# Optimization experiments

Measured on AMD Instinct MI355X. Metric: run time of the kernel, lower is better.

The kernel has to match this reference:

```python
import jax, jax.numpy as jnp
import numpy as np

B, S, D, H = 2, 2048, 1024, 16
DK = D // H


def setup_inputs() -> dict:
    key = jax.random.key(0)
    ks = jax.random.split(key, 7)
    q = jax.random.normal(ks[0], (B, S, D), dtype=jnp.float32)
    k = jax.random.normal(ks[1], (B, S, D), dtype=jnp.float32)
    v = jax.random.normal(ks[2], (B, S, D), dtype=jnp.float32)
    # causal mask (1 = keep, 0 = mask) broadcast over batch/heads
    mask = jnp.tril(jnp.ones((S, S), dtype=jnp.int32))[None, None, :, :]
    scale = 1.0 / np.sqrt(DK)
    W_q = jax.random.normal(ks[3], (D, D), dtype=jnp.float32) * 0.02
    W_k = jax.random.normal(ks[4], (D, D), dtype=jnp.float32) * 0.02
    W_v = jax.random.normal(ks[5], (D, D), dtype=jnp.float32) * 0.02
    W_o = jax.random.normal(ks[6], (D, D), dtype=jnp.float32) * 0.02
    return {"q": q, "k": k, "v": v, "mask": mask,
            "W_q": W_q, "W_k": W_k, "W_v": W_v, "W_o": W_o}


def _split_heads(x):
    # [B, S, D] -> [B, H, S, DK]
    b, s, _ = x.shape
    return x.reshape(b, s, H, DK).transpose(0, 2, 1, 3)


def reference(q, k, v, mask, W_q, W_k, W_v, W_o):
    # nn.Linear(bias=False): y = x @ W.T
    qh = _split_heads(q @ W_q.T)
    kh = _split_heads(k @ W_k.T)
    vh = _split_heads(v @ W_v.T)
    scores = jnp.einsum("bhqd,bhkd->bhqk", qh, kh) / np.sqrt(DK)
    scores = jnp.where(mask == 0, jnp.float32(-1e9), scores)
    attn = jax.nn.softmax(scores, axis=-1)  # dropout p=0 -> identity
    out = jnp.einsum("bhqk,bhkd->bhqd", attn, vh)
    out = out.transpose(0, 2, 1, 3).reshape(q.shape[0], q.shape[1], D)
    return out @ W_o.T
```

## Files before the change

### kernel.cpp

```cpp
#include <hip/hip_runtime.h>
#include <stdint.h>
#include <stddef.h>

typedef __bf16 bf16;
typedef __attribute__((ext_vector_type(4))) __bf16 bf16x4;
typedef __attribute__((ext_vector_type(8))) __bf16 bf16x8;
typedef __attribute__((ext_vector_type(4))) float floatx4;

#define NB 2
#define NS 2048
#define ND 1024
#define NH 16
#define NDK 64
#define NBH (NB*NH)
#define NBS (NB*NS)

__device__ inline void gl2lds16(const bf16* g, bf16* l) {
  __builtin_amdgcn_global_load_lds(
      (const __attribute__((address_space(1))) uint32_t*)(const uint32_t*)(g),
      (__attribute__((address_space(3))) uint32_t*)(uint32_t*)(l),
      16, 0, 0);
}

__global__ __launch_bounds__(256)
void proj_gemm(const float* __restrict__ q, const float* __restrict__ k,
               const float* __restrict__ v,
               const float* __restrict__ Wq, const float* __restrict__ Wk,
               const float* __restrict__ Wv,
               bf16* __restrict__ Qh, bf16* __restrict__ Kh,
               bf16* __restrict__ Vt)
{
  const int z = blockIdx.y, bx = blockIdx.x;
  const int tid = threadIdx.x;
  const int wave = tid >> 6, lane = tid & 63;
  const int quad = lane >> 4, l15 = lane & 15;

  const float *X, *W;
  int m0, n0;
  if (z < 2) { X = z ? k : q;  W = z ? Wk : Wq;
               m0 = (bx >> 3) * 128; n0 = (bx & 7) * 128; }
  else       { X = Wv;         W = v;
               m0 = (bx & 7) * 128;  n0 = (bx >> 3) * 128; }

  __shared__ bf16 As[128 * 32];
  __shared__ bf16 Bs[128 * 32];

  float4 ra[4], rb[4];
#pragma unroll
  for (int it = 0; it < 4; it++) {
    const int lin = it * 256 + tid, row = lin >> 3, ch = lin & 7;
    ra[it] = *(const float4*)(X + (size_t)(m0 + row) * ND + ch * 4);
    rb[it] = *(const float4*)(W + (size_t)(n0 + row) * ND + ch * 4);
  }

  floatx4 acc[4][4];
#pragma unroll
  for (int i = 0; i < 4; i++)
#pragma unroll
    for (int j = 0; j < 4; j++) acc[i][j] = (floatx4)(0.0f);

  const int wm = (wave >> 1) * 64, wn = (wave & 1) * 64;

  for (int k0 = 0; k0 < ND; k0 += 32) {
    __syncthreads();
#pragma unroll
    for (int it = 0; it < 4; it++) {
      const int lin = it * 256 + tid, row = lin >> 3, ch = lin & 7;
      bf16x4 a, b;
      a[0] = (bf16)ra[it].x; a[1] = (bf16)ra[it].y;
      a[2] = (bf16)ra[it].z; a[3] = (bf16)ra[it].w;
      b[0] = (bf16)rb[it].x; b[1] = (bf16)rb[it].y;
      b[2] = (bf16)rb[it].z; b[3] = (bf16)rb[it].w;
      *(bf16x4*)(As + row * 32 + ch * 4) = a;
      *(bf16x4*)(Bs + row * 32 + ch * 4) = b;
    }
    __syncthreads();
    if (k0 + 32 < ND) {
      const int k1 = k0 + 32;
#pragma unroll
      for (int it = 0; it < 4; it++) {
        const int lin = it * 256 + tid, row = lin >> 3, ch = lin & 7;
        ra[it] = *(const float4*)(X + (size_t)(m0 + row) * ND + k1 + ch * 4);
        rb[it] = *(const float4*)(W + (size_t)(n0 + row) * ND + k1 + ch * 4);
      }
    }
    bf16x8 af[4], bfr[4];
#pragma unroll
    for (int i = 0; i < 4; i++)
      af[i] = *(const bf16x8*)(As + (wm + i * 16 + l15) * 32 + quad * 8);
#pragma unroll
    for (int j = 0; j < 4; j++)
      bfr[j] = *(const bf16x8*)(Bs + (wn + j * 16 + l15) * 32 + quad * 8);
#pragma unroll
    for (int i = 0; i < 4; i++)
#pragma unroll
      for (int j = 0; j < 4; j++)
        acc[i][j] = __builtin_amdgcn_mfma_f32_16x16x32_bf16(af[i], bfr[j],
                                                            acc[i][j], 0, 0, 0);
  }

  bf16* O = (z == 0) ? Qh : (z == 1) ? Kh : Vt;
#pragma unroll
  for (int i = 0; i < 4; i++) {
    const int rowb = m0 + wm + i * 16 + quad * 4;
#pragma unroll
    for (int j = 0; j < 4; j++) {
      const int col = n0 + wn + j * 16 + l15;
#pragma unroll
      for (int r = 0; r < 4; r++) {
        const int row = rowb + r;
        const bf16 o = (bf16)acc[i][j][r];
        if (z < 2) {
          const int b = row >> 11, s = row & 2047;
          const int h = col >> 6,  dk = col & 63;
          O[(((size_t)(b * NH + h)) * NS + s) * NDK + dk] = o;
        } else {
          O[((size_t)(col >> 11) * ND + row) * NS + (col & 2047)] = o;
        }
      }
    }
  }
}

__global__ __launch_bounds__(256)
void attn_fwd(const bf16* __restrict__ Qh, const bf16* __restrict__ Kh,
              const bf16* __restrict__ Vt, bf16* __restrict__ Ctx)
{
  const int x = blockIdx.x, bh = blockIdx.y;
  const int tid = threadIdx.x, wave = tid >> 6, lane = tid & 63;
  const int quad = lane >> 4, l15 = lane & 15;

  __shared__ bf16 Ks[2][64 * 64];
  __shared__ bf16 Vs[2][64 * 64];
  __shared__ bf16 Ps[4][16 * 64];

  const size_t qkb = (size_t)bh * NS * NDK;
  const size_t vb  = (size_t)bh * NDK * NS;
  const int b = bh >> 4, h = bh & 15;
  const float C = 0.125f * 1.44269504088896f;

  auto stage = [&](int kt, int buf) {
#pragma unroll
    for (int it = 0; it < 2; it++) {
      const int lin = it * 256 + tid;
      const int row = lin >> 3;
      const int chS = (lin & 7) ^ (row & 7);
      gl2lds16(Kh + qkb + (size_t)(kt * 64 + row) * NDK + chS * 8,
               Ks[buf] + lin * 8);
      gl2lds16(Vt + vb + (size_t)row * NS + kt * 64 + chS * 8,
               Vs[buf] + lin * 8);
    }
  };

  for (int ph = 0; ph < 2; ph++) {
    const int qt = ph ? x : 31 - x;
    const int qrow0 = qt * 64 + wave * 16;

    bf16x8 qf0, qf1;
    {
      const bf16* qp = Qh + qkb + (size_t)(qrow0 + l15) * NDK + quad * 8;
      qf0 = *(const bf16x8*)qp;
      qf1 = *(const bf16x8*)(qp + 32);
    }

    float lsum[4] = {0.0f, 0.0f, 0.0f, 0.0f};
    floatx4 oacc[4];
#pragma unroll
    for (int j = 0; j < 4; j++) oacc[j] = (floatx4)(0.0f);

    __syncthreads();
    stage(0, 0);

    for (int kt = 0; kt <= qt; kt++) {
      const int cur = kt & 1;
      __builtin_amdgcn_s_waitcnt(0);
      __syncthreads();
      if (kt < qt) stage(kt + 1, cur ^ 1);

      const bf16* Ksb = Ks[cur];
      const bf16* Vsb = Vs[cur];

      floatx4 sa[4];
#pragma unroll
      for (int jt = 0; jt < 4; jt++) {
        const int r = jt * 16 + l15;
        const bf16x8 kf0 = *(const bf16x8*)(Ksb + r * 64 + ((quad ^ (r & 7)) << 3));
        const bf16x8 kf1 = *(const bf16x8*)(Ksb + r * 64 + (((4 + quad) ^ (r & 7)) << 3));
        floatx4 zz = (floatx4)(0.0f);
        zz = __builtin_amdgcn_mfma_f32_16x16x32_bf16(qf0, kf0, zz, 0, 0, 0);
        zz = __builtin_amdgcn_mfma_f32_16x16x32_bf16(qf1, kf1, zz, 0, 0, 0);
        sa[jt] = zz;
      }

      const bool diag = (kt == qt);
#pragma unroll
      for (int jt = 0; jt < 4; jt++) {
        const int col = jt * 16 + l15;
#pragma unroll
        for (int r = 0; r < 4; r++) {
          const int row = quad * 4 + r;
          float p = exp2f(sa[jt][r] * C);
          if (diag) p = (kt * 64 + col <= qrow0 + row) ? p : 0.0f;
          lsum[r] += p;
          Ps[wave][row * 64 + ((((col >> 3) ^ (row & 7))) << 3) + (col & 7)] =
              (bf16)p;
        }
      }

#pragma unroll
      for (int ks = 0; ks < 2; ks++) {
        const bf16x8 pf = *(const bf16x8*)(
            &Ps[wave][l15 * 64 + (((ks * 4 + quad) ^ (l15 & 7)) << 3)]);
#pragma unroll
        for (int jt = 0; jt < 4; jt++) {
          const int r = jt * 16 + l15;
          const bf16x8 vf = *(const bf16x8*)(
              Vsb + r * 64 + (((ks * 4 + quad) ^ (r & 7)) << 3));
          oacc[jt] = __builtin_amdgcn_mfma_f32_16x16x32_bf16(pf, vf,
                                                             oacc[jt], 0, 0, 0);
        }
      }
    }

#pragma unroll
    for (int off = 1; off < 16; off <<= 1)
#pragma unroll
      for (int r = 0; r < 4; r++) lsum[r] += __shfl_xor(lsum[r], off, 64);

#pragma unroll
    for (int jt = 0; jt < 4; jt++)
#pragma unroll
      for (int r = 0; r < 4; r++) {
        const int srow = qrow0 + quad * 4 + r;
        Ctx[((size_t)b * NS + srow) * ND + h * 64 + jt * 16 + l15] =
            (bf16)(oacc[jt][r] / lsum[r]);
      }
  }
}

__global__ __launch_bounds__(256)
void out_gemm(const bf16* __restrict__ Ctx, const float* __restrict__ Wo,
              float* __restrict__ out)
{
  const int tid = threadIdx.x;
  const int wave = tid >> 6, lane = tid & 63;
  const int quad = lane >> 4, l15 = lane & 15;
  const int m0 = blockIdx.y * 64, n0 = blockIdx.x * 128;
  const int wm = (wave & 1) * 32, wn = (wave >> 1) * 64;

  __shared__ bf16 As[64 * 32];
  __shared__ bf16 Bs[128 * 32];

  bf16x8 ra;
  float4 rb[4];
  {
    const int row = tid >> 2, ch = tid & 3;
    ra = *(const bf16x8*)(Ctx + (size_t)(m0 + row) * ND + ch * 8);
  }
#pragma unroll
  for (int it = 0; it < 4; it++) {
    const int lin = it * 256 + tid, row = lin >> 3, ch = lin & 7;
    rb[it] = *(const float4*)(Wo + (size_t)(n0 + row) * ND + ch * 4);
  }

  floatx4 acc[2][4];
#pragma unroll
  for (int i = 0; i < 2; i++)
#pragma unroll
    for (int j = 0; j < 4; j++) acc[i][j] = (floatx4)(0.0f);

  for (int k0 = 0; k0 < ND; k0 += 32) {
    __syncthreads();
    {
      const int row = tid >> 2, ch = tid & 3;
      *(bf16x8*)(As + row * 32 + ch * 8) = ra;
    }
#pragma unroll
    for (int it = 0; it < 4; it++) {
      const int lin = it * 256 + tid, row = lin >> 3, ch = lin & 7;
      bf16x4 bb;
      bb[0] = (bf16)rb[it].x; bb[1] = (bf16)rb[it].y;
      bb[2] = (bf16)rb[it].z; bb[3] = (bf16)rb[it].w;
      *(bf16x4*)(Bs + row * 32 + ch * 4) = bb;
    }
    __syncthreads();
    if (k0 + 32 < ND) {
      const int k1 = k0 + 32;
      {
        const int row = tid >> 2, ch = tid & 3;
        ra = *(const bf16x8*)(Ctx + (size_t)(m0 + row) * ND + k1 + ch * 8);
      }
#pragma unroll
      for (int it = 0; it < 4; it++) {
        const int lin = it * 256 + tid, row = lin >> 3, ch = lin & 7;
        rb[it] = *(const float4*)(Wo + (size_t)(n0 + row) * ND + k1 + ch * 4);
      }
    }
    bf16x8 af[2], bfr[4];
#pragma unroll
    for (int i = 0; i < 2; i++)
      af[i] = *(const bf16x8*)(As + (wm + i * 16 + l15) * 32 + quad * 8);
#pragma unroll
    for (int j = 0; j < 4; j++)
      bfr[j] = *(const bf16x8*)(Bs + (wn + j * 16 + l15) * 32 + quad * 8);
#pragma unroll
    for (int i = 0; i < 2; i++)
#pragma unroll
      for (int j = 0; j < 4; j++)
        acc[i][j] = __builtin_amdgcn_mfma_f32_16x16x32_bf16(af[i], bfr[j],
                                                            acc[i][j], 0, 0, 0);
  }

#pragma unroll
  for (int i = 0; i < 2; i++) {
    const int rowb = m0 + wm + i * 16 + quad * 4;
#pragma unroll
    for (int j = 0; j < 4; j++) {
      const int col = n0 + wn + j * 16 + l15;
#pragma unroll
      for (int r = 0; r < 4; r++)
        out[(size_t)(rowb + r) * ND + col] = acc[i][j][r];
    }
  }
}

extern "C" void kernel_launch(void* const* d_in, const int* in_sizes, int n_in,
                              void* d_out, int out_size, void* d_ws, size_t ws_size,
                              hipStream_t stream) {
  const float* q  = (const float*)d_in[0];
  const float* k  = (const float*)d_in[1];
  const float* v  = (const float*)d_in[2];
  const float* Wq = (const float*)d_in[4];
  const float* Wk = (const float*)d_in[5];
  const float* Wv = (const float*)d_in[6];
  const float* Wo = (const float*)d_in[7];
  float* out = (float*)d_out;

  const size_t elems = (size_t)NBS * ND;
  bf16* Qh  = (bf16*)d_ws;
  bf16* Kh  = Qh + elems;
  bf16* Vt  = Kh + elems;
  bf16* Ctx = Vt + elems;

  dim3 blk(256);
  proj_gemm<<<dim3(256, 3), blk, 0, stream>>>(q, k, v, Wq, Wk, Wv, Qh, Kh, Vt);
  attn_fwd<<<dim3(16, NBH), blk, 0, stream>>>(Qh, Kh, Vt, Ctx);
  out_gemm<<<dim3(ND / 128, NBS / 64), blk, 0, stream>>>(Ctx, Wo, out);
}
```

Measured before the change: 258.8 us.

## Pre-convert weights to bf16 and double-buffer GEMM tiles with direct LDS loads

A new kernel converts Wq/Wk/Wv to bf16 once, into workspace that aliases the Ctx buffer. The projection GEMM then streams that bf16 weight tile straight into shared memory with global_load_lds, while the fp32 activation tile is converted in registers. Both projection and output GEMMs now double-buffer their shared tiles so each K step needs one barrier instead of two. They also remap block indices for better L2 locality, and the V projection no longer swaps operands. The costs are an extra kernel launch, extra weight traffic through the workspace, and twice the shared memory per block.

New measurement: 275.8 us. 1.07x slower.

```diff
diff --git a/kernel.cpp b/kernel.cpp
--- a/kernel.cpp
+++ b/kernel.cpp
@@ -23,10 +23,31 @@
 }
 
 __global__ __launch_bounds__(256)
+void convert_w(const float* __restrict__ Wq, const float* __restrict__ Wk,
+               const float* __restrict__ Wv, bf16* __restrict__ Wb)
+{
+  const int z = blockIdx.y;
+  const float* src = (z == 0) ? Wq : (z == 1) ? Wk : Wv;
+  bf16* dst = Wb + (size_t)z * (ND * ND);
+  const size_t off = ((size_t)blockIdx.x * 256 + threadIdx.x) * 32;
+#pragma unroll
+  for (int c = 0; c < 2; c++) {
+    bf16x8 o[2];
+#pragma unroll
+    for (int h = 0; h < 2; h++) {
+      const float4 a = *(const float4*)(src + off + c * 16 + h * 8);
+      const float4 b = *(const float4*)(src + off + c * 16 + h * 8 + 4);
+      o[h][0] = (bf16)a.x; o[h][1] = (bf16)a.y; o[h][2] = (bf16)a.z; o[h][3] = (bf16)a.w;
+      o[h][4] = (bf16)b.x; o[h][5] = (bf16)b.y; o[h][6] = (bf16)b.z; o[h][7] = (bf16)b.w;
+    }
+    *(bf16x8*)(dst + off + c * 16) = o[0];
+    *(bf16x8*)(dst + off + c * 16 + 8) = o[1];
+  }
+}
+
+__global__ __launch_bounds__(256)
 void proj_gemm(const float* __restrict__ q, const float* __restrict__ k,
-               const float* __restrict__ v,
-               const float* __restrict__ Wq, const float* __restrict__ Wk,
-               const float* __restrict__ Wv,
+               const float* __restrict__ v, const bf16* __restrict__ Wb,
                bf16* __restrict__ Qh, bf16* __restrict__ Kh,
                bf16* __restrict__ Vt)
 {
@@ -35,62 +56,76 @@
   const int wave = tid >> 6, lane = tid & 63;
   const int quad = lane >> 4, l15 = lane & 15;
 
-  const float *X, *W;
-  int m0, n0;
-  if (z < 2) { X = z ? k : q;  W = z ? Wk : Wq;
-               m0 = (bx >> 3) * 128; n0 = (bx & 7) * 128; }
-  else       { X = Wv;         W = v;
-               m0 = (bx & 7) * 128;  n0 = (bx >> 3) * 128; }
-
-  __shared__ bf16 As[128 * 32];
-  __shared__ bf16 Bs[128 * 32];
-
-  float4 ra[4], rb[4];
+  const float* X = (z == 0) ? q : (z == 1) ? k : v;
+  const bf16* W = Wb + (size_t)z * (ND * ND);
+  const int c = bx & 7, r = bx >> 3;
+  const int m0 = (c * 4 + (r >> 3)) * 128, n0 = (r & 7) * 128;
+
+  __shared__ bf16 As[2][128 * 32];
+  __shared__ bf16 Bs[2][128 * 32];
+
+  const int arow = tid >> 3, ach = tid & 7;
+  const int brow = tid >> 2, bch = tid & 3;
+
+  floatx4 acc[4][4];
+#pragma unroll
+  for (int i = 0; i < 4; i++)
+#pragma unroll
+    for (int j = 0; j < 4; j++) acc[i][j] = (floatx4)(0.0f);
+
+  const int wm = (wave >> 1) * 64, wn = (wave & 1) * 64;
+
+  float4 ra[4];
+#pragma unroll
+  for (int it = 0; it < 4; it++)
+    ra[it] = *(const float4*)(X + (size_t)(m0 + it * 32 + arow) * ND + ach * 4);
+#pragma unroll
+  for (int it = 0; it < 2; it++)
+    gl2lds16(W + (size_t)(n0 + it * 64 + brow) * ND + bch * 8,
+             Bs[0] + (it * 256 + tid) * 8);
+  __builtin_amdgcn_s_waitcnt(0);
 #pragma unroll
   for (int it = 0; it < 4; it++) {
-    const int lin = it * 256 + tid, row = lin >> 3, ch = lin & 7;
-    ra[it] = *(const float4*)(X + (size_t)(m0 + row) * ND + ch * 4);
-    rb[it] = *(const float4*)(W + (size_t)(n0 + row) * ND + ch * 4);
-  }
-
-  floatx4 acc[4][4];
-#pragma unroll
-  for (int i = 0; i < 4; i++)
-#pragma unroll
-    for (int j = 0; j < 4; j++) acc[i][j] = (floatx4)(0.0f);
-
-  const int wm = (wave >> 1) * 64, wn = (wave & 1) * 64;
-
-  for (int k0 = 0; k0 < ND; k0 += 32) {
+    bf16x4 a;
+    a[0] = (bf16)ra[it].x; a[1] = (bf16)ra[it].y;
+    a[2] = (bf16)ra[it].z; a[3] = (bf16)ra[it].w;
+    *(bf16x4*)(As[0] + (it * 32 + arow) * 32 + ach * 4) = a;
+  }
+#pragma unroll
+  for (int it = 0; it < 4; it++)
+    ra[it] = *(const float4*)(X + (size_t)(m0 + it * 32 + arow) * ND + 32 + ach * 4);
+
+  for (int kk = 0; kk < 32; kk++) {
+    const int cur = kk & 1, nxt = cur ^ 1;
+    __builtin_amdgcn_s_waitcnt(0);
     __syncthreads();
-#pragma unroll
-    for (int it = 0; it < 4; it++) {
-      const int lin = it * 256 + tid, row = lin >> 3, ch = lin & 7;
-      bf16x4 a, b;
-      a[0] = (bf16)ra[it].x; a[1] = (bf16)ra[it].y;
-      a[2] = (bf16)ra[it].z; a[3] = (bf16)ra[it].w;
-      b[0] = (bf16)rb[it].x; b[1] = (bf16)rb[it].y;
-      b[2] = (bf16)rb[it].z; b[3] = (bf16)rb[it].w;
-      *(bf16x4*)(As + row * 32 + ch * 4) = a;
-      *(bf16x4*)(Bs + row * 32 + ch * 4) = b;
-    }
-    __syncthreads();
-    if (k0 + 32 < ND) {
-      const int k1 = k0 + 32;
+    if (kk + 1 < 32) {
+      const int k1 = (kk + 1) * 32;
+#pragma unroll
+      for (int it = 0; it < 2; it++)
+        gl2lds16(W + (size_t)(n0 + it * 64 + brow) * ND + k1 + bch * 8,
+                 Bs[nxt] + (it * 256 + tid) * 8);
 #pragma unroll
       for (int it = 0; it < 4; it++) {
-        const int lin = it * 256 + tid, row = lin >> 3, ch = lin & 7;
-        ra[it] = *(const float4*)(X + (size_t)(m0 + row) * ND + k1 + ch * 4);
-        rb[it] = *(const float4*)(W + (size_t)(n0 + row) * ND + k1 + ch * 4);
+        bf16x4 a;
+        a[0] = (bf16)ra[it].x; a[1] = (bf16)ra[it].y;
+        a[2] = (bf16)ra[it].z; a[3] = (bf16)ra[it].w;
+        *(bf16x4*)(As[nxt] + (it * 32 + arow) * 32 + ach * 4) = a;
+      }
+      if (kk + 2 < 32) {
+        const int k2 = (kk + 2) * 32;
+#pragma unroll
+        for (int it = 0; it < 4; it++)
+          ra[it] = *(const float4*)(X + (size_t)(m0 + it * 32 + arow) * ND + k2 + ach * 4);
       }
     }
     bf16x8 af[4], bfr[4];
 #pragma unroll
     for (int i = 0; i < 4; i++)
-      af[i] = *(const bf16x8*)(As + (wm + i * 16 + l15) * 32 + quad * 8);
+      af[i] = *(const bf16x8*)(As[cur] + (wm + i * 16 + l15) * 32 + quad * 8);
 #pragma unroll
     for (int j = 0; j < 4; j++)
-      bfr[j] = *(const bf16x8*)(Bs + (wn + j * 16 + l15) * 32 + quad * 8);
+      bfr[j] = *(const bf16x8*)(Bs[cur] + (wn + j * 16 + l15) * 32 + quad * 8);
 #pragma unroll
     for (int i = 0; i < 4; i++)
 #pragma unroll
@@ -107,16 +142,15 @@
     for (int j = 0; j < 4; j++) {
       const int col = n0 + wn + j * 16 + l15;
 #pragma unroll
-      for (int r = 0; r < 4; r++) {
-        const int row = rowb + r;
-        const bf16 o = (bf16)acc[i][j][r];
-        if (z < 2) {
-          const int b = row >> 11, s = row & 2047;
-          const int h = col >> 6,  dk = col & 63;
+      for (int rr = 0; rr < 4; rr++) {
+        const int row = rowb + rr;
+        const bf16 o = (bf16)acc[i][j][rr];
+        const int b = row >> 11, s = row & 2047;
+        const int h = col >> 6,  dk = col & 63;
+        if (z < 2)
           O[(((size_t)(b * NH + h)) * NS + s) * NDK + dk] = o;
-        } else {
-          O[((size_t)(col >> 11) * ND + row) * NS + (col & 2047)] = o;
-        }
+        else
+          O[(((size_t)(b * NH + h)) * NDK + dk) * NS + s] = o;
       }
     }
   }
@@ -183,9 +217,9 @@
       floatx4 sa[4];
 #pragma unroll
       for (int jt = 0; jt < 4; jt++) {
-        const int r = jt * 16 + l15;
-        const bf16x8 kf0 = *(const bf16x8*)(Ksb + r * 64 + ((quad ^ (r & 7)) << 3));
-        const bf16x8 kf1 = *(const bf16x8*)(Ksb + r * 64 + (((4 + quad) ^ (r & 7)) << 3));
+        const int rr = jt * 16 + l15;
+        const bf16x8 kf0 = *(const bf16x8*)(Ksb + rr * 64 + ((quad ^ (rr & 7)) << 3));
+        const bf16x8 kf1 = *(const bf16x8*)(Ksb + rr * 64 + (((4 + quad) ^ (rr & 7)) << 3));
         floatx4 zz = (floatx4)(0.0f);
         zz = __builtin_amdgcn_mfma_f32_16x16x32_bf16(qf0, kf0, zz, 0, 0, 0);
         zz = __builtin_amdgcn_mfma_f32_16x16x32_bf16(qf1, kf1, zz, 0, 0, 0);
@@ -197,11 +231,11 @@
       for (int jt = 0; jt < 4; jt++) {
         const int col = jt * 16 + l15;
 #pragma unroll
-        for (int r = 0; r < 4; r++) {
-          const int row = quad * 4 + r;
-          float p = exp2f(sa[jt][r] * C);
+        for (int rr = 0; rr < 4; rr++) {
+          const int row = quad * 4 + rr;
+          float p = exp2f(sa[jt][rr] * C);
           if (diag) p = (kt * 64 + col <= qrow0 + row) ? p : 0.0f;
-          lsum[r] += p;
+          lsum[rr] += p;
           Ps[wave][row * 64 + ((((col >> 3) ^ (row & 7))) << 3) + (col & 7)] =
               (bf16)p;
         }
@@ -213,9 +247,9 @@
             &Ps[wave][l15 * 64 + (((ks * 4 + quad) ^ (l15 & 7)) << 3)]);
 #pragma unroll
         for (int jt = 0; jt < 4; jt++) {
-          const int r = jt * 16 + l15;
+          const int rr = jt * 16 + l15;
           const bf16x8 vf = *(const bf16x8*)(
-              Vsb + r * 64 + (((ks * 4 + quad) ^ (r & 7)) << 3));
+              Vsb + rr * 64 + (((ks * 4 + quad) ^ (rr & 7)) << 3));
           oacc[jt] = __builtin_amdgcn_mfma_f32_16x16x32_bf16(pf, vf,
                                                              oacc[jt], 0, 0, 0);
         }
@@ -225,15 +259,15 @@
 #pragma unroll
     for (int off = 1; off < 16; off <<= 1)
 #pragma unroll
-      for (int r = 0; r < 4; r++) lsum[r] += __shfl_xor(lsum[r], off, 64);
+      for (int rr = 0; rr < 4; rr++) lsum[rr] += __shfl_xor(lsum[rr], off, 64);
 
 #pragma unroll
     for (int jt = 0; jt < 4; jt++)
 #pragma unroll
-      for (int r = 0; r < 4; r++) {
-        const int srow = qrow0 + quad * 4 + r;
+      for (int rr = 0; rr < 4; rr++) {
+        const int srow = qrow0 + quad * 4 + rr;
         Ctx[((size_t)b * NS + srow) * ND + h * 64 + jt * 16 + l15] =
-            (bf16)(oacc[jt][r] / lsum[r]);
+            (bf16)(oacc[jt][rr] / lsum[rr]);
       }
   }
 }
@@ -242,67 +276,70 @@
 void out_gemm(const bf16* __restrict__ Ctx, const float* __restrict__ Wo,
               float* __restrict__ out)
 {
-  const int tid = threadIdx.x;
+  const int bx = blockIdx.x, tid = threadIdx.x;
   const int wave = tid >> 6, lane = tid & 63;
   const int quad = lane >> 4, l15 = lane & 15;
-  const int m0 = blockIdx.y * 64, n0 = blockIdx.x * 128;
+  const int c = bx & 7, r = bx >> 3;
+  const int m0 = (c * 8 + (r >> 3)) * 64, n0 = (r & 7) * 128;
   const int wm = (wave & 1) * 32, wn = (wave >> 1) * 64;
 
-  __shared__ bf16 As[64 * 32];
-  __shared__ bf16 Bs[128 * 32];
-
-  bf16x8 ra;
+  __shared__ bf16 As[2][64 * 32];
+  __shared__ bf16 Bs[2][128 * 32];
+
+  const int arow = tid >> 2, ach = tid & 3;
+  const int brow = tid >> 3, bch = tid & 7;
+
+  floatx4 acc[2][4];
+#pragma unroll
+  for (int i = 0; i < 2; i++)
+#pragma unroll
+    for (int j = 0; j < 4; j++) acc[i][j] = (floatx4)(0.0f);
+
   float4 rb[4];
-  {
-    const int row = tid >> 2, ch = tid & 3;
-    ra = *(const bf16x8*)(Ctx + (size_t)(m0 + row) * ND + ch * 8);
-  }
+  gl2lds16(Ctx + (size_t)(m0 + arow) * ND + ach * 8, As[0] + tid * 8);
+#pragma unroll
+  for (int it = 0; it < 4; it++)
+    rb[it] = *(const float4*)(Wo + (size_t)(n0 + it * 32 + brow) * ND + bch * 4);
+  __builtin_amdgcn_s_waitcnt(0);
 #pragma unroll
   for (int it = 0; it < 4; it++) {
-    const int lin = it * 256 + tid, row = lin >> 3, ch = lin & 7;
-    rb[it] = *(const float4*)(Wo + (size_t)(n0 + row) * ND + ch * 4);
-  }
-
-  floatx4 acc[2][4];
-#pragma unroll
-  for (int i = 0; i < 2; i++)
-#pragma unroll
-    for (int j = 0; j < 4; j++) acc[i][j] = (floatx4)(0.0f);
-
-  for (int k0 = 0; k0 < ND; k0 += 32) {
+    bf16x4 bb;
+    bb[0] = (bf16)rb[it].x; bb[1] = (bf16)rb[it].y;
+    bb[2] = (bf16)rb[it].z; bb[3] = (bf16)rb[it].w;
+    *(bf16x4*)(Bs[0] + (it * 32 + brow) * 32 + bch * 4) = bb;
+  }
+#pragma unroll
+  for (int it = 0; it < 4; it++)
+    rb[it] = *(const float4*)(Wo + (size_t)(n0 + it * 32 + brow) * ND + 32 + bch * 4);
+
+  for (int kk = 0; kk < 32; kk++) {
+    const int cur = kk & 1, nxt = cur ^ 1;
+    __builtin_amdgcn_s_waitcnt(0);
     __syncthreads();
-    {
-      const int row = tid >> 2, ch = tid & 3;
-      *(bf16x8*)(As + row * 32 + ch * 8) = ra;
-    }
-#pragma unroll
-    for (int it = 0; it < 4; it++) {
-      const int lin = it * 256 + tid, row = lin >> 3, ch = lin & 7;
-      bf16x4 bb;
-      bb[0] = (bf16)rb[it].x; bb[1] = (bf16)rb[it].y;
-      bb[2] = (bf16)rb[it].z; bb[3] = (bf16)rb[it].w;
-      *(bf16x4*)(Bs + row * 32 + ch * 4) = bb;
-    }
-    __syncthreads();
-    if (k0 + 32 < ND) {
-      const int k1 = k0 + 32;
-      {
-        const int row = tid >> 2, ch = tid & 3;
-        ra = *(const bf16x8*)(Ctx + (size_t)(m0 + row) * ND + k1 + ch * 8);
-      }
+    if (kk + 1 < 32) {
+      const int k1 = (kk + 1) * 32;
+      gl2lds16(Ctx + (size_t)(m0 + arow) * ND + k1 + ach * 8, As[nxt] + tid * 8);
 #pragma unroll
       for (int it = 0; it < 4; it++) {
-        const int lin = it * 256 + tid, row = lin >> 3, ch = lin & 7;
-        rb[it] = *(const float4*)(Wo + (size_t)(n0 + row) * ND + k1 + ch * 4);
+        bf16x4 bb;
+        bb[0] = (bf16)rb[it].x; bb[1] = (bf16)rb[it].y;
+        bb[2] = (bf16)rb[it].z; bb[3] = (bf16)rb[it].w;
+        *(bf16x4*)(Bs[nxt] + (it * 32 + brow) * 32 + bch * 4) = bb;
+      }
+      if (kk + 2 < 32) {
+        const int k2 = (kk + 2) * 32;
+#pragma unroll
+        for (int it = 0; it < 4; it++)
+          rb[it] = *(const float4*)(Wo + (size_t)(n0 + it * 32 + brow) * ND + k2 + bch * 4);
       }
     }
     bf16x8 af[2], bfr[4];
 #pragma unroll
     for (int i = 0; i < 2; i++)
-      af[i] = *(const bf16x8*)(As + (wm + i * 16 + l15) * 32 + quad * 8);
+      af[i] = *(const bf16x8*)(As[cur] + (wm + i * 16 + l15) * 32 + quad * 8);
 #pragma unroll
     for (int j = 0; j < 4; j++)
-      bfr[j] = *(const bf16x8*)(Bs + (wn + j * 16 + l15) * 32 + quad * 8);
+      bfr[j] = *(const bf16x8*)(Bs[cur] + (wn + j * 16 + l15) * 32 + quad * 8);
 #pragma unroll
     for (int i = 0; i < 2; i++)
 #pragma unroll
@@ -318,8 +355,8 @@
     for (int j = 0; j < 4; j++) {
       const int col = n0 + wn + j * 16 + l15;
 #pragma unroll
-      for (int r = 0; r < 4; r++)
-        out[(size_t)(rowb + r) * ND + col] = acc[i][j][r];
+      for (int rr = 0; rr < 4; rr++)
+        out[(size_t)(rowb + rr) * ND + col] = acc[i][j][rr];
     }
   }
 }
@@ -341,9 +378,11 @@
   bf16* Kh  = Qh + elems;
   bf16* Vt  = Kh + elems;
   bf16* Ctx = Vt + elems;
+  bf16* Wb  = Ctx;
 
   dim3 blk(256);
-  proj_gemm<<<dim3(256, 3), blk, 0, stream>>>(q, k, v, Wq, Wk, Wv, Qh, Kh, Vt);
+  convert_w<<<dim3(128, 3), blk, 0, stream>>>(Wq, Wk, Wv, Wb);
+  proj_gemm<<<dim3(256, 3), blk, 0, stream>>>(q, k, v, Wb, Qh, Kh, Vt);
   attn_fwd<<<dim3(16, NBH), blk, 0, stream>>>(Qh, Kh, Vt, Ctx);
-  out_gemm<<<dim3(ND / 128, NBS / 64), blk, 0, stream>>>(Ctx, Wo, out);
-}
+  out_gemm<<<dim3(512), blk, 0, stream>>>(Ctx, Wo, out);
+}
```
